# Kernel optimization log

Measured on AMD Instinct MI355X. Metric: run time of the kernel, lower is better.

The kernel has to match this reference:

```python
import jax, jax.numpy as jnp
import numpy as np

A = 15           # anchors per location (5 sizes x 3 ratios)
H, W = 200, 320  # feature map size
N = 8            # batch
STRIDE = 4
PRE_NMS = 2000
POST_NMS = 1000
NMS_THRESH = 0.7
MIN_SIZE = 1.0
SCORE_THRESH = 0.0
BBOX_CLIP = float(np.log(1000.0 / 16.0))  # torchvision BoxCoder clamp on dw/dh


def _make_anchors():
    # torchvision-style cell anchors: ratio-major, then sizes, shifted over the grid.
    sizes = np.array([32.0, 64.0, 128.0, 256.0, 512.0])
    ratios = np.array([0.5, 1.0, 2.0])
    h_r = np.sqrt(ratios)
    w_r = 1.0 / h_r
    ws = (w_r[:, None] * sizes[None, :]).reshape(-1)  # [15]
    hs = (h_r[:, None] * sizes[None, :]).reshape(-1)
    base = np.stack([-ws, -hs, ws, hs], axis=1) / 2.0  # [15,4] centered at 0
    sx = np.arange(W) * STRIDE
    sy = np.arange(H) * STRIDE
    yy, xx = np.meshgrid(sy, sx, indexing="ij")
    shifts = np.stack([xx, yy, xx, yy], axis=-1).reshape(-1, 1, 4)  # [H*W,1,4]
    return (shifts + base[None]).reshape(-1, 4).astype(np.float32)  # [H*W*A,4]


def setup_inputs() -> dict:
    key = jax.random.key(0)
    k1, k2 = jax.random.split(key)
    return {
        "box_cls": jax.random.normal(k1, (N, A, H, W), dtype=jnp.float32),
        "box_regression": jax.random.normal(k2, (N, 4 * A, H, W), dtype=jnp.float32),
        "anchors": jnp.asarray(_make_anchors()),
        "img_h": 800,
        "img_w": 1280,
    }


def _decode(deltas, anchors):
    # BoxCoder.decode with weights (1,1,1,1). deltas [N,K,4], anchors [K,4] xyxy.
    wa = anchors[:, 2] - anchors[:, 0]
    ha = anchors[:, 3] - anchors[:, 1]
    cxa = anchors[:, 0] + 0.5 * wa
    cya = anchors[:, 1] + 0.5 * ha
    dx, dy = deltas[..., 0], deltas[..., 1]
    dw = jnp.minimum(deltas[..., 2], BBOX_CLIP)
    dh = jnp.minimum(deltas[..., 3], BBOX_CLIP)
    cx = dx * wa + cxa
    cy = dy * ha + cya
    w = wa * jnp.exp(dw)
    h = ha * jnp.exp(dh)
    return jnp.stack(
        [cx - 0.5 * w, cy - 0.5 * h, cx + 0.5 * w, cy + 0.5 * h], axis=-1
    )


def _nms_keep(boxes, scores):
    # Greedy NMS over boxes sorted by descending score; scores < 0 mark invalid.
    x1, y1, x2, y2 = boxes[:, 0], boxes[:, 1], boxes[:, 2], boxes[:, 3]
    area = (x2 - x1) * (y2 - y1)
    ix = jnp.maximum(0.0, jnp.minimum(x2[:, None], x2[None, :]) - jnp.maximum(x1[:, None], x1[None, :]))
    iy = jnp.maximum(0.0, jnp.minimum(y2[:, None], y2[None, :]) - jnp.maximum(y1[:, None], y1[None, :]))
    inter = ix * iy
    iou = inter / (area[:, None] + area[None, :] - inter)  # [K,K]
    k = boxes.shape[0]
    idx = jnp.arange(k)
    keep0 = scores >= 0.0

    def body(i, keep):
        sup = keep[i] & (iou[i] > NMS_THRESH) & (idx > i)
        return keep & ~sup

    return jax.lax.fori_loop(0, k, body, keep0)


def reference(box_cls, box_regression, anchors, img_h, img_w):
    n = box_cls.shape[0]
    # permute_and_flatten: [N, A*C, H, W] -> [N, H*W*A, C]
    objectness = box_cls.reshape(n, A, 1, H, W).transpose(0, 3, 4, 1, 2).reshape(n, -1)
    deltas = box_regression.reshape(n, A, 4, H, W).transpose(0, 3, 4, 1, 2).reshape(n, -1, 4)
    proposals = _decode(deltas, anchors)  # [N, K, 4]
    # clip to image (single image size for the whole batch)
    fh = jnp.float32(img_h)
    fw = jnp.float32(img_w)
    proposals = jnp.stack(
        [
            jnp.clip(proposals[..., 0], 0.0, fw),
            jnp.clip(proposals[..., 1], 0.0, fh),
            jnp.clip(proposals[..., 2], 0.0, fw),
            jnp.clip(proposals[..., 3], 0.0, fh),
        ],
        axis=-1,
    )
    # pre-NMS top-k per image (single feature level)
    top_s, top_i = jax.lax.top_k(objectness, PRE_NMS)        # [N, PRE]
    boxes = jnp.take_along_axis(proposals, top_i[..., None], axis=1)  # [N, PRE, 4]
    scores = jax.nn.sigmoid(top_s)
    # remove small boxes and low-scoring boxes (mask instead of dynamic shapes)
    ws = boxes[..., 2] - boxes[..., 0]
    hs = boxes[..., 3] - boxes[..., 1]
    valid = (ws >= MIN_SIZE) & (hs >= MIN_SIZE) & (scores >= SCORE_THRESH)
    scores_m = jnp.where(valid, scores, -1.0)
    order = jnp.argsort(-scores_m, axis=1)
    boxes_s = jnp.take_along_axis(boxes, order[..., None], axis=1)
    scores_s = jnp.take_along_axis(scores_m, order, axis=1)
    keep = jax.vmap(_nms_keep)(boxes_s, scores_s)            # [N, PRE] bool
    ks = jnp.where(keep, scores_s, -1.0)
    fs, fi = jax.lax.top_k(ks, POST_NMS)                     # [N, POST]
    fb = jnp.take_along_axis(boxes_s, fi[..., None], axis=1)
    ok = fs >= 0.0
    final_boxes = jnp.where(ok[..., None], fb, 0.0)          # zero-padded, fixed shape
    final_scores = jnp.where(ok, fs, 0.0)
    return final_boxes, final_scores
```

## Files before the change

kernel.cpp:

```cpp
#include <hip/hip_runtime.h>
#include <hip/hip_bf16.h>
#include <stdint.h>

typedef unsigned long long u64;

#define AN 15
#define HH 200
#define WW 320
#define HWSZ (HH*WW)
#define PER (AN*HWSZ)
#define NB 8
#define K_PRE 2000
#define K_POST 1000
#define SORTN 4096
#define SORT2 2048
#define HBINS 4096
#define HBLK 64
#define CBLK 16
#define SLICE (SORTN/CBLK)
#define NMS_TH 0.7f
#define BBOX_CLIP_F 4.135166556742356f

#define PHI(x) ((x) + ((x) >> 3))

__device__ __forceinline__ unsigned keyOfU(unsigned u) {
    return (u & 0x80000000u) ? ~u : (u | 0x80000000u);
}
__device__ __forceinline__ float valOf(unsigned k) {
    unsigned u = (k & 0x80000000u) ? (k ^ 0x80000000u) : ~k;
    return __uint_as_float(u);
}

__global__ __launch_bounds__(256)
void z_init(uint4* __restrict__ z4) {
    z4[blockIdx.x * 256 + threadIdx.x] = make_uint4(0, 0, 0, 0);
}

__global__ __launch_bounds__(256)
void k_hist(const uint4* __restrict__ cls4, unsigned* __restrict__ gh) {
    int n = blockIdx.y;
    __shared__ unsigned lh[2][HBINS];
    for (int b = threadIdx.x; b < HBINS; b += 256) { lh[0][b] = 0; lh[1][b] = 0; }
    __syncthreads();
    unsigned* myh = lh[threadIdx.x & 1];
    const uint4* p = cls4 + (size_t)n * (PER / 4);
    int stride = gridDim.x * 256;
    int i = blockIdx.x * 256 + threadIdx.x;
    for (; i + stride < PER / 4; i += 2 * stride) {
        uint4 a = p[i];
        uint4 b = p[i + stride];
        atomicAdd(&myh[keyOfU(a.x) >> 20], 1u);
        atomicAdd(&myh[keyOfU(a.y) >> 20], 1u);
        atomicAdd(&myh[keyOfU(a.z) >> 20], 1u);
        atomicAdd(&myh[keyOfU(a.w) >> 20], 1u);
        atomicAdd(&myh[keyOfU(b.x) >> 20], 1u);
        atomicAdd(&myh[keyOfU(b.y) >> 20], 1u);
        atomicAdd(&myh[keyOfU(b.z) >> 20], 1u);
        atomicAdd(&myh[keyOfU(b.w) >> 20], 1u);
    }
    if (i < PER / 4) {
        uint4 a = p[i];
        atomicAdd(&myh[keyOfU(a.x) >> 20], 1u);
        atomicAdd(&myh[keyOfU(a.y) >> 20], 1u);
        atomicAdd(&myh[keyOfU(a.z) >> 20], 1u);
        atomicAdd(&myh[keyOfU(a.w) >> 20], 1u);
    }
    __syncthreads();
    unsigned* dst = gh + (size_t)n * HBINS;
    for (int b = threadIdx.x; b < HBINS; b += 256) {
        unsigned v = lh[0][b] + lh[1][b];
        if (v) atomicAdd(&dst[b], v);
    }
}

__global__ __launch_bounds__(1024)
void k_sel(const unsigned* __restrict__ gh, unsigned* __restrict__ selT12,
           unsigned* __restrict__ cntA) {
    int n = blockIdx.x, t = threadIdx.x;
    __shared__ unsigned L[1024];
    uint4 v = *(const uint4*)(gh + (size_t)n * HBINS + 4 * t);
    unsigned sf[5];
    sf[3] = v.w; sf[2] = v.z + sf[3]; sf[1] = v.y + sf[2]; sf[0] = v.x + sf[1];
    L[t] = sf[0];
    __syncthreads();
    for (int off = 1; off < 1024; off <<= 1) {
        unsigned x = L[t] + ((t + off < 1024) ? L[t + off] : 0u);
        __syncthreads(); L[t] = x; __syncthreads();
    }
    unsigned tail = (t < 1023) ? L[t + 1] : 0u;
    sf[0] += tail; sf[1] += tail; sf[2] += tail; sf[3] += tail; sf[4] = tail;
#pragma unroll
    for (int e = 0; e < 4; ++e)
        if (sf[e] >= K_PRE && sf[e + 1] < K_PRE) {
            selT12[n] = 4u * t + e;
            cntA[n] = sf[e + 1];
        }
}

__global__ __launch_bounds__(512)
void k_compact(const uint4* __restrict__ cls4, const unsigned* __restrict__ selT12,
               u64* __restrict__ cand, unsigned* __restrict__ rh) {
    int n = blockIdx.y;
    unsigned t12 = selT12[n];
    __shared__ unsigned cnt;
    __shared__ unsigned rl[HBINS];
    if (threadIdx.x == 0) cnt = 0;
    for (int b = threadIdx.x; b < HBINS; b += 512) rl[b] = 0;
    __syncthreads();
    u64* slice = cand + (size_t)n * SORTN + (size_t)blockIdx.x * SLICE;
    const uint4* p = cls4 + (size_t)n * (PER / 4);
    int stride = gridDim.x * 512;

#define PROC(vv, ii) {                                                        \
        unsigned kk[4] = {keyOfU((vv).x), keyOfU((vv).y), keyOfU((vv).z),     \
                          keyOfU((vv).w)};                                    \
        int i0 = (ii) * 4;                                                    \
        int a = i0 / HWSZ;                                                    \
        int r0 = i0 - a * HWSZ;                                               \
        _Pragma("unroll")                                                     \
        for (int c = 0; c < 4; ++c) {                                         \
            if ((kk[c] >> 20) >= t12) {                                       \
                if ((kk[c] >> 20) == t12)                                     \
                    atomicAdd(&rl[(kk[c] >> 8) & 4095u], 1u);                 \
                unsigned pos = atomicAdd(&cnt, 1u);                           \
                if (pos < SLICE) {                                            \
                    unsigned idx = (unsigned)((r0 + c) * AN + a);             \
                    slice[pos] = ((u64)kk[c] << 32) | (u64)(~idx);            \
                }                                                             \
            }                                                                 \
        }                                                                     \
    }

    int i = blockIdx.x * 512 + threadIdx.x;
    for (; i + 3 * stride < PER / 4; i += 4 * stride) {
        uint4 v0 = p[i];
        uint4 v1 = p[i + stride];
        uint4 v2 = p[i + 2 * stride];
        uint4 v3 = p[i + 3 * stride];
        PROC(v0, i) PROC(v1, i + stride) PROC(v2, i + 2 * stride) PROC(v3, i + 3 * stride)
    }
    for (; i < PER / 4; i += stride) { uint4 v0 = p[i]; PROC(v0, i) }
#undef PROC

    __syncthreads();
    unsigned c0 = cnt; if (c0 > SLICE) c0 = SLICE;
    for (unsigned t = c0 + threadIdx.x; t < SLICE; t += 512) slice[t] = 0ull;
    unsigned* dst = rh + (size_t)n * HBINS;
    for (int b = threadIdx.x; b < HBINS; b += 512) {
        unsigned v = rl[b];
        if (v) atomicAdd(&dst[b], v);
    }
}

__global__ __launch_bounds__(1024)
void k_sel2(const unsigned* __restrict__ rh, const unsigned* __restrict__ selT12,
            const unsigned* __restrict__ cntA, unsigned* __restrict__ selT24) {
    int n = blockIdx.x, t = threadIdx.x;
    __shared__ unsigned L[1024];
    uint4 v = *(const uint4*)(rh + (size_t)n * HBINS + 4 * t);
    unsigned sf[5];
    sf[3] = v.w; sf[2] = v.z + sf[3]; sf[1] = v.y + sf[2]; sf[0] = v.x + sf[1];
    L[t] = sf[0];
    __syncthreads();
    for (int off = 1; off < 1024; off <<= 1) {
        unsigned x = L[t] + ((t + off < 1024) ? L[t + off] : 0u);
        __syncthreads(); L[t] = x; __syncthreads();
    }
    unsigned tail = (t < 1023) ? L[t + 1] : 0u;
    sf[0] += tail; sf[1] += tail; sf[2] += tail; sf[3] += tail; sf[4] = tail;
    unsigned need = K_PRE - cntA[n];
#pragma unroll
    for (int e = 0; e < 4; ++e)
        if (sf[e] >= need && sf[e + 1] < need)
            selT24[n] = (selT12[n] << 12) | (4u * t + e);
}

__global__ __launch_bounds__(256)
void k_sort(u64* __restrict__ cand, const unsigned* __restrict__ selT24) {
    int n = blockIdx.x;
    int tid = threadIdx.x;
    __shared__ u64 sb[PHI(SORT2 - 1) + 1];
    __shared__ unsigned cnt;
    if (tid == 0) cnt = 0;
    __syncthreads();
    unsigned T24 = selT24[n];
    u64* src = cand + (size_t)n * SORTN;

    for (int s = 0; s < SORTN / 256; ++s) {
        u64 e = src[tid + s * 256];
        if ((unsigned)(e >> 40) >= T24) {
            unsigned pos = atomicAdd(&cnt, 1u);
            if (pos < SORT2) sb[PHI((int)pos)] = e;
        }
    }
    __syncthreads();
    unsigned c0 = cnt; if (c0 > SORT2) c0 = SORT2;
    for (unsigned t = c0 + tid; t < SORT2; t += 256) sb[PHI((int)t)] = 0ull;
    __syncthreads();

    u64 r[8];
#define CE(a_, b_, d_) { bool sw_ = (d_) ? (r[a_] < r[b_]) : (r[a_] > r[b_]); \
                         if (sw_) { u64 t_ = r[a_]; r[a_] = r[b_]; r[b_] = t_; } }

    {
#pragma unroll
        for (int e = 0; e < 8; ++e) r[e] = sb[9 * tid + e];
        CE(0, 1, true)  CE(2, 3, false) CE(4, 5, true)  CE(6, 7, false)
        CE(0, 2, true)  CE(1, 3, true)  CE(4, 6, false) CE(5, 7, false)
        CE(0, 1, true)  CE(2, 3, true)  CE(4, 5, false) CE(6, 7, false)
#pragma unroll
        for (int e = 0; e < 8; ++e) sb[9 * tid + e] = r[e];
        __syncthreads();
    }

    for (int k = 8; k <= SORT2; k <<= 1) {
        for (int j = k >> 1; j >= 8; j >>= 1) {
#pragma unroll
            for (int s = 0; s < 4; ++s) {
                int c = tid + s * 256;
                int i = ((c & ~(j - 1)) << 1) | (c & (j - 1));
                int p = i | j;
                bool dir = (i & k) == 0;
                u64 a = sb[PHI(i)], b = sb[PHI(p)];
                bool sw = dir ? (a < b) : (a > b);
                if (sw) { sb[PHI(i)] = b; sb[PHI(p)] = a; }
            }
            __syncthreads();
        }
        {
            bool d = ((8 * tid) & k) == 0;
#pragma unroll
            for (int e = 0; e < 8; ++e) r[e] = sb[9 * tid + e];
            CE(0, 4, d) CE(1, 5, d) CE(2, 6, d) CE(3, 7, d)
            CE(0, 2, d) CE(1, 3, d) CE(4, 6, d) CE(5, 7, d)
            CE(0, 1, d) CE(2, 3, d) CE(4, 5, d) CE(6, 7, d)
#pragma unroll
            for (int e = 0; e < 8; ++e) sb[9 * tid + e] = r[e];
            __syncthreads();
        }
    }
#undef CE

    for (int t = tid; t < SORT2; t += 256)
        src[t] = sb[PHI(t)];
}

__global__ __launch_bounds__(1024)
void k_decode(const float* __restrict__ reg, const float* __restrict__ anchors,
              const int* __restrict__ pih, const int* __restrict__ piw,
              const u64* __restrict__ cand,
              float* __restrict__ boxes_s, float* __restrict__ scores_s) {
    int n = blockIdx.x;
    int tid = threadIdx.x;
    float fh = (float)(*pih);
    float fw = (float)(*piw);

    float bx[2][4]; float sc[2]; int pred[2];
#pragma unroll
    for (int q = 0; q < 2; ++q) {
        int t = tid + 1024 * q;
        pred[q] = 0; sc[q] = -1.0f;
        bx[q][0] = bx[q][1] = bx[q][2] = bx[q][3] = 0.f;
        if (t < K_PRE) {
            u64 e = cand[(size_t)n * SORTN + t];
            unsigned key = (unsigned)(e >> 32);
            unsigned idx = ~((unsigned)e);
            float v = valOf(key);
            float s = 1.0f / (1.0f + expf(-v));
            int a = (int)(idx % AN);
            int rr = (int)(idx / AN);
            size_t base = ((size_t)(n * AN + a) * 4) * HWSZ + rr;
            float dx = reg[base];
            float dy = reg[base + HWSZ];
            float dw = reg[base + 2 * (size_t)HWSZ];
            float dh = reg[base + 3 * (size_t)HWSZ];
            float4 an4 = ((const float4*)anchors)[idx];
            float wa = an4.z - an4.x, ha = an4.w - an4.y;
            float cxa = an4.x + 0.5f * wa, cya = an4.y + 0.5f * ha;
            dw = fminf(dw, BBOX_CLIP_F); dh = fminf(dh, BBOX_CLIP_F);
            float cx = dx * wa + cxa, cy = dy * ha + cya;
            float w = wa * expf(dw), h = ha * expf(dh);
            float x1 = cx - 0.5f * w, y1 = cy - 0.5f * h;
            float x2 = cx + 0.5f * w, y2 = cy + 0.5f * h;
            x1 = fminf(fmaxf(x1, 0.f), fw);
            y1 = fminf(fmaxf(y1, 0.f), fh);
            x2 = fminf(fmaxf(x2, 0.f), fw);
            y2 = fminf(fmaxf(y2, 0.f), fh);
            bool valid = ((x2 - x1) >= 1.0f) && ((y2 - y1) >= 1.0f);
            bx[q][0] = x1; bx[q][1] = y1; bx[q][2] = x2; bx[q][3] = y2;
            sc[q] = s; pred[q] = valid ? 1 : 0;
        }
    }

    __shared__ u64 ww[32];
    __shared__ int wpfx[33];
    int lane = tid & 63, wid = tid >> 6;
#pragma unroll
    for (int q = 0; q < 2; ++q) {
        u64 bal = __ballot(pred[q] != 0);
        if (lane == 0) ww[wid + 16 * q] = bal;
    }
    __syncthreads();
    if (tid == 0) {
        int s = 0;
#pragma unroll
        for (int w2 = 0; w2 < 32; ++w2) { wpfx[w2] = s; s += (int)__popcll(ww[w2]); }
        wpfx[32] = s;
    }
    __syncthreads();
    int V = wpfx[32];

#pragma unroll
    for (int q = 0; q < 2; ++q) {
        int t = tid + 1024 * q;
        if (t < K_PRE) {
            int wi = t >> 6;
            int before = wpfx[wi] + (int)__popcll(ww[wi] & ((1ull << (unsigned)lane) - 1ull));
            int pos = pred[q] ? before : (V + (t - before));
            float4 b4; b4.x = bx[q][0]; b4.y = bx[q][1]; b4.z = bx[q][2]; b4.w = bx[q][3];
            ((float4*)boxes_s)[(size_t)n * K_PRE + pos] = b4;
            scores_s[(size_t)n * K_PRE + pos] = pred[q] ? sc[q] : -1.0f;
        }
    }
}

__global__ __launch_bounds__(64)
void k_maskT(const float* __restrict__ boxes_s, u64* __restrict__ maskT) {
    int n = blockIdx.y;
    int p = blockIdx.x;
    int lane = threadIdx.x;
    int cb = (int)((sqrtf(8.0f * (float)p + 1.0f) - 1.0f) * 0.5f);
    while ((cb + 1) * (cb + 2) / 2 <= p) ++cb;
    while (cb * (cb + 1) / 2 > p) --cb;
    int rb = p - cb * (cb + 1) / 2;

    __shared__ float rx1[64], ry1[64], rx2[64], ry2[64], rar[64];
    int c = cb * 64 + lane;
    bool cok = c < K_PRE;
    float4 c4; c4.x = c4.y = c4.z = c4.w = 0.f;
    if (cok) c4 = ((const float4*)boxes_s)[(size_t)n * K_PRE + c];
    float areaC = (c4.z - c4.x) * (c4.w - c4.y);

    int r = rb * 64 + lane;
    float4 r4; r4.x = r4.y = r4.z = r4.w = 0.f;
    if (r < K_PRE) r4 = ((const float4*)boxes_s)[(size_t)n * K_PRE + r];
    rx1[lane] = r4.x; ry1[lane] = r4.y; rx2[lane] = r4.z; ry2[lane] = r4.w;
    rar[lane] = (r4.z - r4.x) * (r4.w - r4.y);
    __syncthreads();

    u64 bits = 0;
    int bmax = 0;
    if (cok) { bmax = c - rb * 64; if (bmax > 64) bmax = 64; }
    for (int b = 0; b < bmax; ++b) {
        float ix = fminf(c4.z, rx2[b]) - fmaxf(c4.x, rx1[b]); ix = fmaxf(ix, 0.f);
        float iy = fminf(c4.w, ry2[b]) - fmaxf(c4.y, ry1[b]); iy = fmaxf(iy, 0.f);
        float inter = ix * iy;
        float iou = inter / (rar[b] + areaC - inter);
        if (iou > NMS_TH) bits |= (1ull << b);
    }
    maskT[((size_t)n * 32 + rb) * 2048 + c] = bits;
}

__global__ __launch_bounds__(64)
void k_scanT(const u64* __restrict__ maskT, const float* __restrict__ boxes_s,
             const float* __restrict__ scores_s, float* __restrict__ out) {
    int n = blockIdx.x;
    int lane = threadIdx.x;
    __shared__ float ls[2048];
    __shared__ u64 keptw[32];
    for (int i = lane; i < 2048; i += 64)
        ls[i] = (i < K_PRE) ? scores_s[(size_t)n * K_PRE + i] : -1.0f;
    if (lane < 32) keptw[lane] = 0ull;
    __syncthreads();

    const u64* mb = maskT + (size_t)n * 32 * 2048;
    int kept_total = 0;

    u64 wv[32];
#pragma unroll
    for (int rb = 0; rb < 32; ++rb) wv[rb] = mb[(size_t)rb * 2048 + lane];

    for (int f = 0; f < 32; ++f) {
        int c = f * 64 + lane;

        u64 wn[32];
        if (f < 31) {
            int cn = c + 64;
#pragma unroll
            for (int rb = 0; rb < 32; ++rb) wn[rb] = mb[(size_t)rb * 2048 + cn];
        }

        u64 hit = 0;
#pragma unroll
        for (int rb = 0; rb < 32; ++rb) hit |= (wv[rb] & keptw[rb]);
        bool ext = hit != 0ull;
        u64 diag = wv[f];

        bool v = (ls[c] >= 0.0f) && !ext;
        u64 kept = __ballot(v);
        while (true) {
            u64 nk = __ballot(v && ((diag & kept) == 0ull));
            if (nk == kept) break;
            kept = nk;
        }

        if ((kept >> lane) & 1ull) {
            int rank = kept_total + (int)__popcll(kept & ((1ull << lane) - 1ull));
            if (rank < K_POST) {
                float4 b4 = ((const float4*)boxes_s)[(size_t)n * K_PRE + c];
                ((float4*)out)[(size_t)n * K_POST + rank] = b4;
                out[(size_t)NB * K_POST * 4 + (size_t)n * K_POST + rank] = ls[c];
            }
        }
        kept_total += (int)__popcll(kept);
        if (lane == 0) keptw[f] = kept;
        if (kept_total >= K_POST || f == 31) break;
#pragma unroll
        for (int rb = 0; rb < 32; ++rb) wv[rb] = wn[rb];
    }

    int start = (kept_total < K_POST) ? kept_total : K_POST;
    float4 z4; z4.x = z4.y = z4.z = z4.w = 0.f;
    for (int rk = start + lane; rk < K_POST; rk += 64) {
        ((float4*)out)[(size_t)n * K_POST + rk] = z4;
        out[(size_t)NB * K_POST * 4 + (size_t)n * K_POST + rk] = 0.f;
    }
}

extern "C" void kernel_launch(void* const* d_in, const int* in_sizes, int n_in,
                              void* d_out, int out_size, void* d_ws, size_t ws_size,
                              hipStream_t stream) {
    const float* cls     = (const float*)d_in[0];
    const float* regr    = (const float*)d_in[1];
    const float* anchors = (const float*)d_in[2];
    const int*   pih     = (const int*)d_in[3];
    const int*   piw     = (const int*)d_in[4];
    float* out = (float*)d_out;

    char* w = (char*)d_ws;
    u64*      maskT   = (u64*)(w + 0);
    unsigned* gh      = (unsigned*)(w + 4194304);
    unsigned* rh      = (unsigned*)(w + 4325376);
    unsigned* selT12  = (unsigned*)(w + 4456448);
    unsigned* cntA    = (unsigned*)(w + 4456480);
    unsigned* selT24  = (unsigned*)(w + 4456512);
    u64*      cand    = (u64*)(w + 4456576);
    float*    boxes_s = (float*)(w + 4718720);
    float*    scores_s= (float*)(w + 4974720);

    z_init<<<64, 256, 0, stream>>>((uint4*)gh);
    k_hist<<<dim3(HBLK, NB), 256, 0, stream>>>((const uint4*)cls, gh);
    k_sel<<<NB, 1024, 0, stream>>>(gh, selT12, cntA);
    k_compact<<<dim3(CBLK, NB), 512, 0, stream>>>((const uint4*)cls, selT12, cand, rh);
    k_sel2<<<NB, 1024, 0, stream>>>(rh, selT12, cntA, selT24);
    k_sort<<<NB, 256, 0, stream>>>(cand, selT24);
    k_decode<<<NB, 1024, 0, stream>>>(regr, anchors, pih, piw,
                                      cand, boxes_s, scores_s);
    k_maskT<<<dim3(528, NB), 64, 0, stream>>>(boxes_s, maskT);
    k_scanT<<<NB, 64, 0, stream>>>(maskT, boxes_s, scores_s, out);
    (void)in_sizes; (void)n_in; (void)ws_size;
}
```

Baseline: 134.4 us.

## Restrict histogram to top key range, drop refine pass, sort full candidate buffer

The first histogram now counts only keys whose top 12 bits lie at or above a floor, which cuts shared-memory atomics for most elements. A fallback histogram and select pass run only when the threshold is not found in that range. The second-level refine histogram and its select kernel are removed, and the sort instead runs a bitonic sort over the full 4096-entry candidate buffer with 512 threads. This trades one kernel and many atomics for a larger in-LDS sort, and it depends on each compaction slice not overflowing its fixed capacity.

```diff
diff --git a/kernel.cpp b/kernel.cpp
--- a/kernel.cpp
+++ b/kernel.cpp
@@ -13,13 +13,14 @@
 #define K_PRE 2000
 #define K_POST 1000
 #define SORTN 4096
-#define SORT2 2048
 #define HBINS 4096
 #define HBLK 64
 #define CBLK 16
 #define SLICE (SORTN/CBLK)
 #define NMS_TH 0.7f
 #define BBOX_CLIP_F 4.135166556742356f
+#define FLOOR12 3072u
+#define SENT 0xFFFFFFFFu
 
 #define PHI(x) ((x) + ((x) >> 3))
 
@@ -32,50 +33,43 @@
 }
 
 __global__ __launch_bounds__(256)
-void z_init(uint4* __restrict__ z4) {
-    z4[blockIdx.x * 256 + threadIdx.x] = make_uint4(0, 0, 0, 0);
+void z_init(uint4* __restrict__ gh4, unsigned* __restrict__ selT12) {
+    gh4[blockIdx.x * 256 + threadIdx.x] = make_uint4(0, 0, 0, 0);
+    if (blockIdx.x == 0 && threadIdx.x < NB) selT12[threadIdx.x] = SENT;
 }
 
 __global__ __launch_bounds__(256)
-void k_hist(const uint4* __restrict__ cls4, unsigned* __restrict__ gh) {
+void k_histF(const uint4* __restrict__ cls4, unsigned* __restrict__ gh) {
     int n = blockIdx.y;
-    __shared__ unsigned lh[2][HBINS];
-    for (int b = threadIdx.x; b < HBINS; b += 256) { lh[0][b] = 0; lh[1][b] = 0; }
-    __syncthreads();
-    unsigned* myh = lh[threadIdx.x & 1];
+    __shared__ unsigned lh[HBINS];
+    for (int b = threadIdx.x; b < HBINS; b += 256) lh[b] = 0;
+    __syncthreads();
     const uint4* p = cls4 + (size_t)n * (PER / 4);
     int stride = gridDim.x * 256;
     int i = blockIdx.x * 256 + threadIdx.x;
+#define H4(vv) { unsigned k0 = keyOfU((vv).x) >> 20, k1 = keyOfU((vv).y) >> 20, \
+                          k2 = keyOfU((vv).z) >> 20, k3 = keyOfU((vv).w) >> 20; \
+        if (k0 >= FLOOR12) atomicAdd(&lh[k0], 1u);                              \
+        if (k1 >= FLOOR12) atomicAdd(&lh[k1], 1u);                              \
+        if (k2 >= FLOOR12) atomicAdd(&lh[k2], 1u);                              \
+        if (k3 >= FLOOR12) atomicAdd(&lh[k3], 1u); }
     for (; i + stride < PER / 4; i += 2 * stride) {
         uint4 a = p[i];
         uint4 b = p[i + stride];
-        atomicAdd(&myh[keyOfU(a.x) >> 20], 1u);
-        atomicAdd(&myh[keyOfU(a.y) >> 20], 1u);
-        atomicAdd(&myh[keyOfU(a.z) >> 20], 1u);
-        atomicAdd(&myh[keyOfU(a.w) >> 20], 1u);
-        atomicAdd(&myh[keyOfU(b.x) >> 20], 1u);
-        atomicAdd(&myh[keyOfU(b.y) >> 20], 1u);
-        atomicAdd(&myh[keyOfU(b.z) >> 20], 1u);
-        atomicAdd(&myh[keyOfU(b.w) >> 20], 1u);
-    }
-    if (i < PER / 4) {
-        uint4 a = p[i];
-        atomicAdd(&myh[keyOfU(a.x) >> 20], 1u);
-        atomicAdd(&myh[keyOfU(a.y) >> 20], 1u);
-        atomicAdd(&myh[keyOfU(a.z) >> 20], 1u);
-        atomicAdd(&myh[keyOfU(a.w) >> 20], 1u);
-    }
+        H4(a) H4(b)
+    }
+    if (i < PER / 4) { uint4 a = p[i]; H4(a) }
+#undef H4
     __syncthreads();
     unsigned* dst = gh + (size_t)n * HBINS;
     for (int b = threadIdx.x; b < HBINS; b += 256) {
-        unsigned v = lh[0][b] + lh[1][b];
+        unsigned v = lh[b];
         if (v) atomicAdd(&dst[b], v);
     }
 }
 
 __global__ __launch_bounds__(1024)
-void k_sel(const unsigned* __restrict__ gh, unsigned* __restrict__ selT12,
-           unsigned* __restrict__ cntA) {
+void k_sel(const unsigned* __restrict__ gh, unsigned* __restrict__ selT12) {
     int n = blockIdx.x, t = threadIdx.x;
     __shared__ unsigned L[1024];
     uint4 v = *(const uint4*)(gh + (size_t)n * HBINS + 4 * t);
@@ -91,21 +85,65 @@
     sf[0] += tail; sf[1] += tail; sf[2] += tail; sf[3] += tail; sf[4] = tail;
 #pragma unroll
     for (int e = 0; e < 4; ++e)
-        if (sf[e] >= K_PRE && sf[e + 1] < K_PRE) {
-            selT12[n] = 4u * t + e;
-            cntA[n] = sf[e + 1];
-        }
+        if (sf[e] >= K_PRE && sf[e + 1] < K_PRE) selT12[n] = 4u * t + e;
+}
+
+__global__ __launch_bounds__(256)
+void k_histR(const uint4* __restrict__ cls4, unsigned* __restrict__ gh,
+             const unsigned* __restrict__ selT12) {
+    int n = blockIdx.y;
+    if (selT12[n] != SENT) return;
+    __shared__ unsigned lh[HBINS];
+    for (int b = threadIdx.x; b < HBINS; b += 256) lh[b] = 0;
+    __syncthreads();
+    const uint4* p = cls4 + (size_t)n * (PER / 4);
+    int stride = gridDim.x * 256;
+#define H4(vv) { unsigned k0 = keyOfU((vv).x) >> 20, k1 = keyOfU((vv).y) >> 20, \
+                          k2 = keyOfU((vv).z) >> 20, k3 = keyOfU((vv).w) >> 20; \
+        if (k0 < FLOOR12) atomicAdd(&lh[k0], 1u);                               \
+        if (k1 < FLOOR12) atomicAdd(&lh[k1], 1u);                               \
+        if (k2 < FLOOR12) atomicAdd(&lh[k2], 1u);                               \
+        if (k3 < FLOOR12) atomicAdd(&lh[k3], 1u); }
+    for (int i = blockIdx.x * 256 + threadIdx.x; i < PER / 4; i += stride) {
+        uint4 a = p[i]; H4(a)
+    }
+#undef H4
+    __syncthreads();
+    unsigned* dst = gh + (size_t)n * HBINS;
+    for (int b = threadIdx.x; b < HBINS; b += 256) {
+        unsigned v = lh[b];
+        if (v) atomicAdd(&dst[b], v);
+    }
+}
+
+__global__ __launch_bounds__(1024)
+void k_selR(const unsigned* __restrict__ gh, unsigned* __restrict__ selT12) {
+    int n = blockIdx.x, t = threadIdx.x;
+    if (selT12[n] != SENT) return;
+    __shared__ unsigned L[1024];
+    uint4 v = *(const uint4*)(gh + (size_t)n * HBINS + 4 * t);
+    unsigned sf[5];
+    sf[3] = v.w; sf[2] = v.z + sf[3]; sf[1] = v.y + sf[2]; sf[0] = v.x + sf[1];
+    L[t] = sf[0];
+    __syncthreads();
+    for (int off = 1; off < 1024; off <<= 1) {
+        unsigned x = L[t] + ((t + off < 1024) ? L[t + off] : 0u);
+        __syncthreads(); L[t] = x; __syncthreads();
+    }
+    unsigned tail = (t < 1023) ? L[t + 1] : 0u;
+    sf[0] += tail; sf[1] += tail; sf[2] += tail; sf[3] += tail; sf[4] = tail;
+#pragma unroll
+    for (int e = 0; e < 4; ++e)
+        if (sf[e] >= K_PRE && sf[e + 1] < K_PRE) selT12[n] = 4u * t + e;
 }
 
 __global__ __launch_bounds__(512)
 void k_compact(const uint4* __restrict__ cls4, const unsigned* __restrict__ selT12,
-               u64* __restrict__ cand, unsigned* __restrict__ rh) {
+               u64* __restrict__ cand) {
     int n = blockIdx.y;
     unsigned t12 = selT12[n];
     __shared__ unsigned cnt;
-    __shared__ unsigned rl[HBINS];
     if (threadIdx.x == 0) cnt = 0;
-    for (int b = threadIdx.x; b < HBINS; b += 512) rl[b] = 0;
     __syncthreads();
     u64* slice = cand + (size_t)n * SORTN + (size_t)blockIdx.x * SLICE;
     const uint4* p = cls4 + (size_t)n * (PER / 4);
@@ -120,8 +158,6 @@
         _Pragma("unroll")                                                     \
         for (int c = 0; c < 4; ++c) {                                         \
             if ((kk[c] >> 20) >= t12) {                                       \
-                if ((kk[c] >> 20) == t12)                                     \
-                    atomicAdd(&rl[(kk[c] >> 8) & 4095u], 1u);                 \
                 unsigned pos = atomicAdd(&cnt, 1u);                           \
                 if (pos < SLICE) {                                            \
                     unsigned idx = (unsigned)((r0 + c) * AN + a);             \
@@ -145,66 +181,22 @@
     __syncthreads();
     unsigned c0 = cnt; if (c0 > SLICE) c0 = SLICE;
     for (unsigned t = c0 + threadIdx.x; t < SLICE; t += 512) slice[t] = 0ull;
-    unsigned* dst = rh + (size_t)n * HBINS;
-    for (int b = threadIdx.x; b < HBINS; b += 512) {
-        unsigned v = rl[b];
-        if (v) atomicAdd(&dst[b], v);
-    }
-}
-
-__global__ __launch_bounds__(1024)
-void k_sel2(const unsigned* __restrict__ rh, const unsigned* __restrict__ selT12,
-            const unsigned* __restrict__ cntA, unsigned* __restrict__ selT24) {
-    int n = blockIdx.x, t = threadIdx.x;
-    __shared__ unsigned L[1024];
-    uint4 v = *(const uint4*)(rh + (size_t)n * HBINS + 4 * t);
-    unsigned sf[5];
-    sf[3] = v.w; sf[2] = v.z + sf[3]; sf[1] = v.y + sf[2]; sf[0] = v.x + sf[1];
-    L[t] = sf[0];
-    __syncthreads();
-    for (int off = 1; off < 1024; off <<= 1) {
-        unsigned x = L[t] + ((t + off < 1024) ? L[t + off] : 0u);
-        __syncthreads(); L[t] = x; __syncthreads();
-    }
-    unsigned tail = (t < 1023) ? L[t + 1] : 0u;
-    sf[0] += tail; sf[1] += tail; sf[2] += tail; sf[3] += tail; sf[4] = tail;
-    unsigned need = K_PRE - cntA[n];
-#pragma unroll
-    for (int e = 0; e < 4; ++e)
-        if (sf[e] >= need && sf[e + 1] < need)
-            selT24[n] = (selT12[n] << 12) | (4u * t + e);
-}
-
-__global__ __launch_bounds__(256)
-void k_sort(u64* __restrict__ cand, const unsigned* __restrict__ selT24) {
+}
+
+__global__ __launch_bounds__(512)
+void k_sort(u64* __restrict__ cand) {
     int n = blockIdx.x;
     int tid = threadIdx.x;
-    __shared__ u64 sb[PHI(SORT2 - 1) + 1];
-    __shared__ unsigned cnt;
-    if (tid == 0) cnt = 0;
-    __syncthreads();
-    unsigned T24 = selT24[n];
-    u64* src = cand + (size_t)n * SORTN;
-
-    for (int s = 0; s < SORTN / 256; ++s) {
-        u64 e = src[tid + s * 256];
-        if ((unsigned)(e >> 40) >= T24) {
-            unsigned pos = atomicAdd(&cnt, 1u);
-            if (pos < SORT2) sb[PHI((int)pos)] = e;
-        }
-    }
-    __syncthreads();
-    unsigned c0 = cnt; if (c0 > SORT2) c0 = SORT2;
-    for (unsigned t = c0 + tid; t < SORT2; t += 256) sb[PHI((int)t)] = 0ull;
-    __syncthreads();
-
+    __shared__ u64 sb[PHI(SORTN - 1) + 1];
     u64 r[8];
+
 #define CE(a_, b_, d_) { bool sw_ = (d_) ? (r[a_] < r[b_]) : (r[a_] > r[b_]); \
                          if (sw_) { u64 t_ = r[a_]; r[a_] = r[b_]; r[b_] = t_; } }
 
     {
-#pragma unroll
-        for (int e = 0; e < 8; ++e) r[e] = sb[9 * tid + e];
+        const u64* src = cand + (size_t)n * SORTN + 8 * tid;
+#pragma unroll
+        for (int e = 0; e < 8; ++e) r[e] = src[e];
         CE(0, 1, true)  CE(2, 3, false) CE(4, 5, true)  CE(6, 7, false)
         CE(0, 2, true)  CE(1, 3, true)  CE(4, 6, false) CE(5, 7, false)
         CE(0, 1, true)  CE(2, 3, true)  CE(4, 5, false) CE(6, 7, false)
@@ -213,11 +205,11 @@
         __syncthreads();
     }
 
-    for (int k = 8; k <= SORT2; k <<= 1) {
+    for (int k = 8; k <= SORTN; k <<= 1) {
         for (int j = k >> 1; j >= 8; j >>= 1) {
 #pragma unroll
             for (int s = 0; s < 4; ++s) {
-                int c = tid + s * 256;
+                int c = tid + s * 512;
                 int i = ((c & ~(j - 1)) << 1) | (c & (j - 1));
                 int p = i | j;
                 bool dir = (i & k) == 0;
@@ -241,8 +233,8 @@
     }
 #undef CE
 
-    for (int t = tid; t < SORT2; t += 256)
-        src[t] = sb[PHI(t)];
+    for (int t = tid; t < 2048; t += 512)
+        cand[(size_t)n * SORTN + t] = sb[PHI(t)];
 }
 
 __global__ __launch_bounds__(1024)
@@ -368,8 +360,9 @@
     int lane = threadIdx.x;
     __shared__ float ls[2048];
     __shared__ u64 keptw[32];
-    for (int i = lane; i < 2048; i += 64)
-        ls[i] = (i < K_PRE) ? scores_s[(size_t)n * K_PRE + i] : -1.0f;
+    for (int i = lane; i < 512; i += 64)
+        ((float4*)ls)[i] = ((const float4*)(scores_s + (size_t)n * K_PRE))[i];
+    if (lane < 48) ls[2000 + lane] = -1.0f;
     if (lane < 32) keptw[lane] = 0ull;
     __syncthreads();
 
@@ -440,20 +433,18 @@
     char* w = (char*)d_ws;
     u64*      maskT   = (u64*)(w + 0);
     unsigned* gh      = (unsigned*)(w + 4194304);
-    unsigned* rh      = (unsigned*)(w + 4325376);
-    unsigned* selT12  = (unsigned*)(w + 4456448);
-    unsigned* cntA    = (unsigned*)(w + 4456480);
-    unsigned* selT24  = (unsigned*)(w + 4456512);
-    u64*      cand    = (u64*)(w + 4456576);
-    float*    boxes_s = (float*)(w + 4718720);
-    float*    scores_s= (float*)(w + 4974720);
-
-    z_init<<<64, 256, 0, stream>>>((uint4*)gh);
-    k_hist<<<dim3(HBLK, NB), 256, 0, stream>>>((const uint4*)cls, gh);
-    k_sel<<<NB, 1024, 0, stream>>>(gh, selT12, cntA);
-    k_compact<<<dim3(CBLK, NB), 512, 0, stream>>>((const uint4*)cls, selT12, cand, rh);
-    k_sel2<<<NB, 1024, 0, stream>>>(rh, selT12, cntA, selT24);
-    k_sort<<<NB, 256, 0, stream>>>(cand, selT24);
+    unsigned* selT12  = (unsigned*)(w + 4325376);
+    u64*      cand    = (u64*)(w + 4325408);
+    float*    boxes_s = (float*)(w + 4587552);
+    float*    scores_s= (float*)(w + 4843552);
+
+    z_init<<<32, 256, 0, stream>>>((uint4*)gh, selT12);
+    k_histF<<<dim3(HBLK, NB), 256, 0, stream>>>((const uint4*)cls, gh);
+    k_sel<<<NB, 1024, 0, stream>>>(gh, selT12);
+    k_histR<<<dim3(HBLK, NB), 256, 0, stream>>>((const uint4*)cls, gh, selT12);
+    k_selR<<<NB, 1024, 0, stream>>>(gh, selT12);
+    k_compact<<<dim3(CBLK, NB), 512, 0, stream>>>((const uint4*)cls, selT12, cand);
+    k_sort<<<NB, 512, 0, stream>>>(cand);
     k_decode<<<NB, 1024, 0, stream>>>(regr, anchors, pih, piw,
                                       cand, boxes_s, scores_s);
     k_maskT<<<dim3(528, NB), 64, 0, stream>>>(boxes_s, maskT);
```

Measured after the change: 127.4 us. 5.2% less time.
